# Performance work log

Measured on AMD Instinct MI355X. Metric: run time of the kernel, lower is better.

## Reference

```python
import jax, jax.numpy as jnp
from jax import lax
import numpy as np

AXIS = 16      # axis_neuron
N_TYPES = 2    # number of atom types


def _mlp(x, Ws, bs):
    for W, b in zip(Ws, bs):
        x = jnp.tanh(x @ W + b)
    return x


def _forward(sym, dx, dy, dz, types,
             fw0, fb0, fw1, fb1, fw2, fb2,
             gw0, gb0, gw1, gb1, gw2, gb2, gwo, gbo):
    # sym/dx/dy/dz: (B, N, SEL, 4); types: (B, N) int
    N, SEL = sym.shape[1], sym.shape[2]

    def frame_fn(R, DX, DY, DZ, ty):
        E_atoms = jnp.zeros((N,), R.dtype)
        F = jnp.zeros((N, 3), R.dtype)
        for t in range(N_TYPES):  # loop over small fixed set of atom types
            mask = (ty == t).astype(R.dtype)            # (N,)
            cnt = jnp.maximum(mask.sum(), 1.0)
            m3 = mask[:, None, None]
            sji = R[:, :, 0:1]
            xyz = R[:, :, 1:4]
            ns = cnt * SEL
            nx = ns * 3.0
            s_avg = (sji * m3).sum() / ns
            x_avg = (xyz * m3).sum() / nx
            s_avg2 = ((sji ** 2) * m3).sum() / ns
            x_avg2 = ((xyz ** 2) * m3).sum() / nx
            avg2 = jnp.stack([s_avg2, x_avg2, x_avg2, x_avg2])
            avg1 = jnp.stack([s_avg, x_avg, x_avg, x_avg])
            std = jnp.sqrt(jnp.maximum(avg2 - avg1 ** 2, 0.0)) + 1e-8
            avg = jnp.stack([s_avg, 0.0 * s_avg, 0.0 * s_avg, 0.0 * s_avg])
            avg = lax.stop_gradient(avg)   # torch computes stats under no_grad
            std = lax.stop_gradient(std)
            Rn = (R - avg) / std
            DXn = DX / std
            DYn = DY / std
            DZn = DZ / std

            def etot(Rn_):
                s = Rn_[:, :, 0:1]                                  # (N, SEL, 1)
                G = _mlp(s, [fw0[t], fw1[t], fw2[t]], [fb0[t], fb1[t], fb2[t]])  # (N, SEL, M)
                RG = jnp.einsum('nsf,nsm->nfm', Rn_, G)             # (N, 4, M)
                GRRG = jnp.einsum('nfm,nfa->nma', RG, RG[:, :, :AXIS]).reshape(N, -1)  # (N, M*AXIS)
                denom = cnt * GRRG.shape[1]
                mu = (GRRG * mask[:, None]).sum() / denom
                mu2 = ((GRRG ** 2) * mask[:, None]).sum() / denom
                sd = jnp.sqrt(jnp.maximum(mu2 - mu ** 2, 0.0)) + 1e-8
                h = _mlp((GRRG - mu) / sd,
                         [gw0[t], gw1[t], gw2[t]], [gb0[t], gb1[t], gb2[t]])
                e = (h @ gwo[t] + gbo[t])[:, 0]                     # (N,)
                return (e * mask).sum(), e

            (Et, e_atoms), dR = jax.value_and_grad(etot, has_aux=True)(Rn)
            E_atoms = E_atoms + e_atoms * mask
            Fx = (dR * DXn).sum(axis=(1, 2))
            Fy = (dR * DYn).sum(axis=(1, 2))
            Fz = (dR * DZn).sum(axis=(1, 2))
            # "DO NOT forget to multiply -1 for F!!!"
            F = F - jnp.stack([Fx, Fy, Fz], axis=1) * mask[:, None]
        return E_atoms.sum(), F

    return jax.vmap(frame_fn)(sym, dx, dy, dz, types)


def setup_inputs() -> dict:
    key = jax.random.key(0)
    ks = jax.random.split(key, 24)
    B, N, SEL = 4, 1024, 128
    M = 100                     # filter_neuron[-1]
    FIT_IN = AXIS * M           # 1600
    d = {}
    d['sym'] = jax.random.normal(ks[0], (B, N, SEL, 4), jnp.float32)
    d['dx'] = jax.random.normal(ks[1], (B, N, SEL, 4), jnp.float32)
    d['dy'] = jax.random.normal(ks[2], (B, N, SEL, 4), jnp.float32)
    d['dz'] = jax.random.normal(ks[3], (B, N, SEL, 4), jnp.float32)
    d['types'] = jax.random.randint(ks[4], (B, N), 0, N_TYPES, jnp.int32)

    def w(k, shape):
        return jax.random.normal(k, shape, jnp.float32) / np.float32(np.sqrt(shape[-2]))

    def b(k, shape):
        return 0.1 * jax.random.normal(k, shape, jnp.float32)

    d['fw0'] = w(ks[5], (N_TYPES, 1, 25));      d['fb0'] = b(ks[6], (N_TYPES, 25))
    d['fw1'] = w(ks[7], (N_TYPES, 25, 50));     d['fb1'] = b(ks[8], (N_TYPES, 50))
    d['fw2'] = w(ks[9], (N_TYPES, 50, M));      d['fb2'] = b(ks[10], (N_TYPES, M))
    d['gw0'] = w(ks[11], (N_TYPES, FIT_IN, 240)); d['gb0'] = b(ks[12], (N_TYPES, 240))
    d['gw1'] = w(ks[13], (N_TYPES, 240, 240));  d['gb1'] = b(ks[14], (N_TYPES, 240))
    d['gw2'] = w(ks[15], (N_TYPES, 240, 240));  d['gb2'] = b(ks[16], (N_TYPES, 240))
    d['gwo'] = w(ks[17], (N_TYPES, 240, 1));    d['gbo'] = b(ks[18], (N_TYPES, 1))
    return d


def reference(sym, dx, dy, dz, types,
              fw0, fb0, fw1, fb1, fw2, fb2,
              gw0, gb0, gw1, gb1, gw2, gb2, gwo, gbo):
    return _forward(sym, dx, dy, dz, types,
                    fw0, fb0, fw1, fb1, fw2, fb2,
                    gw0, gb0, gw1, gb1, gw2, gb2, gwo, gbo)
```

## Files before the change

### kernel.cpp

```cpp
#include <hip/hip_runtime.h>

#define NBATCH 4
#define NATOM 1024
#define NSEL 128
#define H1 25
#define H2 50
#define HM 100
#define AX 16
#define GF 1600
#define FI 240
#define NT 2
#define NGRP64 18

#define WS_STATS_RAW 0
#define WS_STATS_FIN 64
#define WS_MUSD_RAW 128
#define WS_MUSD_FIN 144
#define WS_S_RAW 176
#define WS_CTR 192
#define WS_EBUF 256
#define WS_IDX (WS_EBUF + NBATCH*NATOM)
#define WS_G (WS_IDX + NBATCH*1152)
#define WS_P (WS_G + (size_t)NBATCH*NATOM*GF)
#define WS_BP0  (WS_P + (size_t)NBATCH*NATOM*GF)
#define WS_BP1  (WS_BP0 + (size_t)NT*15*50*256)
#define WS_BP2  (WS_BP1 + (size_t)NT*15*8*256)
#define WS_BPT2 (WS_BP2 + (size_t)NT*15*8*256)
#define WS_BPT1 (WS_BPT2 + (size_t)NT*15*8*256)
#define WS_BPT0 (WS_BPT1 + (size_t)NT*15*8*256)
#define WS_FW1T (WS_BPT0 + (size_t)NT*100*8*256)
#define WS_FW2T (WS_FW1T + (size_t)NT*H2*H1)
#define WS_RGB (WS_FW2T + (size_t)NT*HM*H2)
#define WS_GTB (WS_RGB + (size_t)NBATCH*NATOM*HM*4)
#define WS_GTB_UNITS ((size_t)NBATCH*NATOM*(HM/2)*NSEL)
#define WS_BF1B  (WS_GTB + WS_GTB_UNITS)
#define WS_BW2TB (WS_BF1B + (size_t)NT*1024)
#define WS_BW1TB (WS_BW2TB + (size_t)NT*4096)
#define WS_BF2B  (WS_BW1TB + (size_t)NT*1024)
#define WS_END   (WS_BF2B + (size_t)NT*3584)

#define GSTR 108

typedef __attribute__((ext_vector_type(8))) short bf16x8;
typedef __attribute__((ext_vector_type(4))) float f32x4;

__device__ __forceinline__ float ftanh(float x){
  float e = __expf(2.0f*x);
  return 1.0f - 2.0f/(e+1.0f);
}
__device__ __forceinline__ unsigned short f2bf(float x){
  unsigned b=__float_as_uint(x); b += 0x7FFF + ((b>>16)&1); return (unsigned short)(b>>16);
}
__device__ __forceinline__ float bf2f(unsigned short h){ return __uint_as_float(((unsigned)h)<<16); }
__device__ __forceinline__ float bflo(unsigned u){ return __uint_as_float(u<<16); }
__device__ __forceinline__ float bfhi(unsigned u){ return __uint_as_float(u & 0xFFFF0000u); }
__device__ __forceinline__ unsigned packbf(float a, float b){
  return (unsigned)f2bf(a) | ((unsigned)f2bf(b)<<16);
}

__device__ __forceinline__ float wave_sum(float v){
#pragma unroll
  for(int o=32;o>0;o>>=1) v += __shfl_down(v,o,64);
  return v;
}
__device__ __forceinline__ float block_sum2(float v, float* red){
  v = wave_sum(v);
  __syncthreads();
  if((threadIdx.x&63)==0) red[threadIdx.x>>6]=v;
  __syncthreads();
  return red[0]+red[1];
}
__device__ __forceinline__ float block_sum4(float v, float* red){
  v = wave_sum(v);
  __syncthreads();
  if((threadIdx.x&63)==0) red[threadIdx.x>>6]=v;
  __syncthreads();
  return red[0]+red[1]+red[2]+red[3];
}

__global__ void __launch_bounds__(256) k_transpose(const float* __restrict__ gw0,
    const float* __restrict__ gw1, const float* __restrict__ gw2,
    const float* __restrict__ fw1, const float* __restrict__ fw2, float* __restrict__ ws){
  const int cB0 = NT*15*50*256;
  const int cB1 = NT*15*8*256;
  const int cT0 = NT*100*8*256;
  const int c6 = NT*H2*H1, c7 = NT*HM*H2;
  const int total = cB0 + 4*cB1 + cT0 + c6 + c7;
  unsigned* wsu = (unsigned*)ws;
  for(int i = blockIdx.x*blockDim.x + threadIdx.x; i < total; i += gridDim.x*blockDim.x){
    if(i < cB0 + 4*cB1 + cT0){
      int base, NKs; const float* W; int KK; int mode; int t;
      int ii = i;
      if(ii < cB0){ base=WS_BP0; NKs=50; KK=1600; mode=0; t = ii/(15*50*256); ii -= t*(15*50*256); W = gw0 + (size_t)t*GF*FI; }
      else if(ii < cB0+cB1){ ii-=cB0; base=WS_BP1; NKs=8; KK=240; mode=0; t = ii/(15*8*256); ii -= t*(15*8*256); W = gw1 + t*FI*FI; }
      else if(ii < cB0+2*cB1){ ii-=cB0+cB1; base=WS_BP2; NKs=8; KK=240; mode=0; t = ii/(15*8*256); ii -= t*(15*8*256); W = gw2 + t*FI*FI; }
      else if(ii < cB0+3*cB1){ ii-=cB0+2*cB1; base=WS_BPT2; NKs=8; KK=240; mode=1; t = ii/(15*8*256); ii -= t*(15*8*256); W = gw2 + t*FI*FI; }
      else if(ii < cB0+4*cB1){ ii-=cB0+3*cB1; base=WS_BPT1; NKs=8; KK=240; mode=1; t = ii/(15*8*256); ii -= t*(15*8*256); W = gw1 + t*FI*FI; }
      else { ii-=cB0+4*cB1; base=WS_BPT0; NKs=8; KK=240; mode=2; t = ii/(100*8*256); ii -= t*(100*8*256); W = gw0 + (size_t)t*GF*FI; }
      int d = ii & 3;
      int lane = (ii>>2) & 63;
      int rem = ii >> 8;
      int ks = rem % NKs;
      int ntile = rem / NKs;
      int n = ntile*16 + (lane&15);
      int k0 = ks*32 + ((lane>>4)&3)*8 + 2*d;
      float v0, v1;
      if(mode==0){
        v0 = (k0   < KK) ? W[(size_t)(k0  )*FI + n] : 0.f;
        v1 = (k0+1 < KK) ? W[(size_t)(k0+1)*FI + n] : 0.f;
      } else if(mode==1){
        v0 = (k0   < KK) ? W[n*FI + k0  ] : 0.f;
        v1 = (k0+1 < KK) ? W[n*FI + k0+1] : 0.f;
      } else {
        v0 = (k0   < KK) ? W[(size_t)n*FI + k0  ] : 0.f;
        v1 = (k0+1 < KK) ? W[(size_t)n*FI + k0+1] : 0.f;
      }
      int telems = (base==WS_BP0) ? 15*50*256 : (base==WS_BPT0 ? 100*8*256 : 15*8*256);
      wsu[base + (size_t)t*telems + ii] = packbf(v0, v1);
    } else if(i < cB0 + 4*cB1 + cT0 + c6){
      int ii = i - (cB0+4*cB1+cT0); int t = ii/(H2*H1); int rem = ii - t*(H2*H1);
      int j = rem/H1; int k = rem - j*H1;
      ws[WS_FW1T + ii] = fw1[t*H1*H2 + k*H2 + j];
    } else {
      int ii = i - (cB0+4*cB1+cT0+c6); int t = ii/(HM*H2); int rem = ii - t*(HM*H2);
      int m = rem/H2; int j = rem - m*H2;
      ws[WS_FW2T + ii] = fw2[t*H2*HM + j*HM + m];
    }
  }
}

__global__ void __launch_bounds__(256) k_packf(const float* __restrict__ fw1,
    const float* __restrict__ fw2, float* __restrict__ ws){
  unsigned* wsu = (unsigned*)ws;
  const int c1 = NT*1024, c2 = NT*4096, c3 = NT*1024, c4 = NT*3584;
  const int total = c1 + c2 + c3 + c4;
  for(int i = blockIdx.x*blockDim.x + threadIdx.x; i < total; i += gridDim.x*blockDim.x){
    if(i < c1){
      int t = i/1024; int ii = i - t*1024;
      int nt = ii>>8; int lane = (ii>>2)&63; int d = ii&3;
      int n = nt*16 + (lane&15);
      int k0 = ((lane>>4)&3)*8 + 2*d;
      float v0 = (k0   < H1 && n < H2) ? fw1[t*H1*H2 + (k0  )*H2 + n] : 0.f;
      float v1 = (k0+1 < H1 && n < H2) ? fw1[t*H1*H2 + (k0+1)*H2 + n] : 0.f;
      wsu[WS_BF1B + i] = packbf(v0, v1);
    } else if(i < c1 + c2){
      int ii = i - c1; int t = ii/4096; ii -= t*4096;
      int nt = ii>>10; int ks = (ii>>8)&3; int lane = (ii>>2)&63; int d = ii&3;
      int n = nt*16 + (lane&15);
      int k0 = ks*32 + ((lane>>4)&3)*8 + 2*d;
      float v0 = (k0   < HM && n < H2) ? fw2[t*H2*HM + n*HM + k0  ] : 0.f;
      float v1 = (k0+1 < HM && n < H2) ? fw2[t*H2*HM + n*HM + k0+1] : 0.f;
      wsu[WS_BW2TB + ii + t*4096] = packbf(v0, v1);
    } else if(i < c1 + c2 + c3){
      int ii = i - c1 - c2; int t = ii/1024; ii -= t*1024;
      int nt = ii>>9; int ks = (ii>>8)&1; int lane = (ii>>2)&63; int d = ii&3;
      int n = nt*16 + (lane&15);
      int k0 = ks*32 + ((lane>>4)&3)*8 + 2*d;
      float v0 = (k0   < H2 && n < H1) ? fw1[t*H1*H2 + n*H2 + k0  ] : 0.f;
      float v1 = (k0+1 < H2 && n < H1) ? fw1[t*H1*H2 + n*H2 + k0+1] : 0.f;
      wsu[WS_BW1TB + ii + t*1024] = packbf(v0, v1);
    } else {
      int ii = i - c1 - c2 - c3; int t = ii/3584; ii -= t*3584;
      int nt = ii>>9; int ks = (ii>>8)&1; int lane = (ii>>2)&63; int d = ii&3;
      int n = nt*16 + (lane&15);
      int k0 = ks*32 + ((lane>>4)&3)*8 + 2*d;
      float v0 = (k0   < H2 && n < HM) ? fw2[t*H2*HM + (k0  )*HM + n] : 0.f;
      float v1 = (k0+1 < H2 && n < HM) ? fw2[t*H2*HM + (k0+1)*HM + n] : 0.f;
      wsu[WS_BF2B + ii + t*3584] = packbf(v0, v1);
    }
  }
}

__global__ void __launch_bounds__(256) k_stats(const float* __restrict__ sym,
    const int* __restrict__ types, float* __restrict__ ws){
  const int b = blockIdx.y;
  const int n0 = blockIdx.x * 64;
  const float* R = sym + ((size_t)b*NATOM + n0)*NSEL*4;
  const int* ty = types + b*NATOM;
  float ss0=0,ss20=0,xs0=0,xs20=0,ss1=0,ss21=0,xs1=0,xs21=0,c0=0,c1=0;
  for(int idx=threadIdx.x; idx<64*NSEL*4; idx+=256){
    int a = idx >> 9;
    int t = ty[n0+a];
    float v = R[idx];
    bool iss = (idx&3)==0;
    if(t==0){ if(iss){ss0+=v;ss20+=v*v;} else {xs0+=v;xs20+=v*v;} }
    else    { if(iss){ss1+=v;ss21+=v*v;} else {xs1+=v;xs21+=v*v;} }
  }
  if(threadIdx.x<64){ if(ty[n0+threadIdx.x]==0) c0=1.f; else c1=1.f; }
  ss0=wave_sum(ss0); ss20=wave_sum(ss20); xs0=wave_sum(xs0); xs20=wave_sum(xs20); c0=wave_sum(c0);
  ss1=wave_sum(ss1); ss21=wave_sum(ss21); xs1=wave_sum(xs1); xs21=wave_sum(xs21); c1=wave_sum(c1);
  if((threadIdx.x&63)==0){
    float* r0 = ws + WS_STATS_RAW + (b*2+0)*8;
    float* r1 = ws + WS_STATS_RAW + (b*2+1)*8;
    atomicAdd(r0+0,c0); atomicAdd(r0+1,ss0); atomicAdd(r0+2,ss20); atomicAdd(r0+3,xs0); atomicAdd(r0+4,xs20);
    atomicAdd(r1+0,c1); atomicAdd(r1+1,ss1); atomicAdd(r1+2,ss21); atomicAdd(r1+3,xs1); atomicAdd(r1+4,xs21);
  }
}

__global__ void k_fin_stats(float* ws){
  int i = threadIdx.x;
  if(i<8){
    float* raw = ws + WS_STATS_RAW + i*8;
    float cntf = fmaxf(raw[0], 1.f);
    float ns = cntf * (float)NSEL;
    float s_avg = raw[1]/ns, s_avg2 = raw[2]/ns;
    float x_avg = raw[3]/(ns*3.f), x_avg2 = raw[4]/(ns*3.f);
    float std_s = sqrtf(fmaxf(s_avg2 - s_avg*s_avg, 0.f)) + 1e-8f;
    float std_x = sqrtf(fmaxf(x_avg2 - x_avg*x_avg, 0.f)) + 1e-8f;
    float* fin = ws + WS_STATS_FIN + i*8;
    fin[0]=s_avg; fin[1]=1.f/std_s; fin[2]=1.f/std_x; fin[3]=cntf; fin[4]=raw[0];
  }
}

__global__ void k_index(const int* __restrict__ types, float* __restrict__ ws){
  int b = blockIdx.x;
  int rc0 = (int)ws[WS_STATS_FIN + (b*2)*8 + 4];
  int pad0 = (rc0+63)&~63;
  int* ctr = (int*)ws + WS_CTR;
  int* idx = (int*)ws + WS_IDX;
  for(int n=threadIdx.x;n<NATOM;n+=256){
    int t = types[b*NATOM+n];
    int pos = atomicAdd(&ctr[b*2+t],1);
    idx[b*1152 + (t ? pad0+pos : pos)] = n;
  }
}

__global__ void __launch_bounds__(128) k_fwdm(const float* __restrict__ sym, const int* __restrict__ types,
    const float* __restrict__ fw0,const float* __restrict__ fb0,
    const float* __restrict__ fb1,const float* __restrict__ fb2,
    float* __restrict__ ws){
  extern __shared__ char fraw[];
  float* Rn4 = (float*)fraw;
  float* RG4 = (float*)(fraw + 2048);
  float* red = (float*)(fraw + 3648);
  unsigned short* a2F = (unsigned short*)(fraw + 3680);
  unsigned* a2Fu = (unsigned*)(fraw + 3680);
  unsigned* a1L = (unsigned*)(fraw + 20576);
  unsigned short* Gl = (unsigned short*)(fraw + 20576);

  const int bid = blockIdx.x;
  const int b = bid >> 10;
  int t = types[bid];
  t = __builtin_amdgcn_readfirstlane(t);
  const float* fin = ws + WS_STATS_FIN + (b*2+t)*8;
  const float avg_s = fin[0], inv_ss = fin[1], inv_sx = fin[2];
  const int s = threadIdx.x;
  const int wave = s>>6, lane = s&63, lw = lane&15, lg = lane>>4;

  const float* W0 = fw0 + t*H1; const float* B0 = fb0 + t*H1;
  const float* B1 = fb1 + t*H2; const float* B2 = fb2 + t*HM;
  const unsigned* wsu = (const unsigned*)ws;
  const bf16x8* BF1 = (const bf16x8*)(wsu + WS_BF1B) + t*4*64;
  const bf16x8* BF2 = (const bf16x8*)(wsu + WS_BF2B) + t*14*64;

  float4 R4 = *(const float4*)&sym[(size_t)bid*NSEL*4 + s*4];
  float rn0 = (R4.x-avg_s)*inv_ss, rn1 = R4.y*inv_sx, rn2 = R4.z*inv_sx, rn3 = R4.w*inv_sx;
  *(float4*)&Rn4[s*4] = make_float4(rn0,rn1,rn2,rn3);

  {
    float a1r[H1];
#pragma unroll
    for(int kk=0;kk<H1;kk++) a1r[kk] = ftanh(rn0*W0[kk] + B0[kk]);
    unsigned* rw = a1L + s*17;
#pragma unroll
    for(int q=0;q<12;q++) rw[q] = packbf(a1r[2*q], a1r[2*q+1]);
    rw[12] = packbf(a1r[24], 0.f);
    rw[13]=0; rw[14]=0; rw[15]=0; rw[16]=0;
  }
  __syncthreads();

  const f32x4 fz = {0.f,0.f,0.f,0.f};
  for(int nt=0;nt<4;nt++){
    f32x4 acc[4];
#pragma unroll
    for(int mt=0;mt<4;mt++){
      int MT = wave*4 + mt;
      bf16x8 af = *(const bf16x8*)&a1L[(MT*16+lw)*17 + lg*4];
      acc[mt] = __builtin_amdgcn_mfma_f32_16x16x32_bf16(af, BF1[nt*64+lane], fz, 0,0,0);
    }
    int col = nt*16 + lw;
    float bias = (col<H2) ? B1[col] : 0.f;
#pragma unroll
    for(int mt=0;mt<4;mt++)
#pragma unroll
      for(int r=0;r<4;r++){
        int rw = (wave*4+mt)*16 + lg*4 + r;
        float v = (col<H2) ? ftanh(acc[mt][r] + bias) : 0.f;
        a2F[rw*66 + col] = f2bf(v);
      }
  }
  __syncthreads();
  for(int nt=0;nt<7;nt++){
    f32x4 acc[4];
#pragma unroll
    for(int mt=0;mt<4;mt++) acc[mt] = fz;
    for(int ks=0;ks<2;ks++){
#pragma unroll
      for(int mt=0;mt<4;mt++){
        int MT = wave*4 + mt;
        bf16x8 af = *(const bf16x8*)&a2Fu[(MT*16+lw)*33 + ks*16 + lg*4];
        acc[mt] = __builtin_amdgcn_mfma_f32_16x16x32_bf16(af, BF2[(nt*2+ks)*64+lane], acc[mt], 0,0,0);
      }
    }
    int col = nt*16 + lw;
    if(col < HM){
      float bias = B2[col];
#pragma unroll
      for(int mt=0;mt<4;mt++)
#pragma unroll
        for(int r=0;r<4;r++){
          int rw = (wave*4+mt)*16 + lg*4 + r;
          Gl[rw*GSTR + col] = f2bf(ftanh(acc[mt][r] + bias));
        }
    }
  }
  __syncthreads();
  if(s < HM){
    const int m = s;
    float a0=0,b0=0,c0=0,d0=0;
    for(int sn=0;sn<NSEL;sn++){
      float4 rn = *(const float4*)&Rn4[sn*4];
      float g = bf2f(Gl[sn*GSTR+m]);
      a0 += rn.x*g; b0 += rn.y*g; c0 += rn.z*g; d0 += rn.w*g;
    }
    *(float4*)&RG4[m*4] = make_float4(a0,b0,c0,d0);
  }
  __syncthreads();
  for(int i=s;i<HM*4;i+=128) ws[WS_RGB + (size_t)bid*(HM*4) + i] = RG4[i];
  {
    unsigned* GT = (unsigned*)ws + WS_GTB + (size_t)bid*((HM/2)*NSEL);
    for(int i=s;i<(HM/2)*NSEL;i+=128){
      int mp = i >> 7, ss = i & 127;
      GT[i] = *(const unsigned*)&Gl[ss*GSTR + 2*mp];
    }
  }
  float lsum=0,lsum2=0;
  float* gout = ws + WS_G + (size_t)bid*GF;
  for(int i=s;i<GF;i+=128){
    int m=i>>4, a=i&15;
    float4 rm = *(const float4*)&RG4[m*4];
    float4 ra = *(const float4*)&RG4[a*4];
    float gv = rm.x*ra.x + rm.y*ra.y + rm.z*ra.z + rm.w*ra.w;
    gout[i]=gv; lsum+=gv; lsum2+=gv*gv;
  }
  lsum = block_sum2(lsum, red);
  lsum2 = block_sum2(lsum2, red);
  if(s==0){
    atomicAdd(&ws[WS_MUSD_RAW + (b*2+t)*2 + 0], lsum);
    atomicAdd(&ws[WS_MUSD_RAW + (b*2+t)*2 + 1], lsum2);
  }
}

__global__ void __launch_bounds__(128) k_fwd(const float* __restrict__ sym, const int* __restrict__ types,
    const float* __restrict__ fw0,const float* __restrict__ fb0,
    const float* __restrict__ fb1,const float* __restrict__ fb2,
    float* __restrict__ ws){
  __shared__ float Rn4[NSEL*4];
  __shared__ unsigned short Gl[NSEL*GSTR];
  __shared__ float RG4[HM*4];
  __shared__ float red[8];

  const int bid = blockIdx.x;
  const int b = bid >> 10;
  int t = types[bid];
  t = __builtin_amdgcn_readfirstlane(t);
  const float* fin = ws + WS_STATS_FIN + (b*2+t)*8;
  const float avg_s = fin[0], inv_ss = fin[1], inv_sx = fin[2];
  const int s = threadIdx.x;

  const float* W0 = fw0 + t*H1; const float* B0 = fb0 + t*H1;
  const float* B1 = fb1 + t*H2; const float* B2 = fb2 + t*HM;
  const float* W1T = ws + WS_FW1T + t*H2*H1;
  const float* W2T = ws + WS_FW2T + t*HM*H2;

  float4 R4 = *(const float4*)&sym[(size_t)bid*NSEL*4 + s*4];
  float rn0 = (R4.x-avg_s)*inv_ss, rn1 = R4.y*inv_sx, rn2 = R4.z*inv_sx, rn3 = R4.w*inv_sx;
  *(float4*)&Rn4[s*4] = make_float4(rn0,rn1,rn2,rn3);

  float a1[H1];
#pragma unroll
  for(int k=0;k<H1;k++) a1[k] = ftanh(rn0*W0[k] + B0[k]);
  float a2[H2];
#pragma unroll
  for(int j=0;j<H2;j++){
    float acc = B1[j];
    const float* wr = W1T + j*H1;
#pragma unroll
    for(int k=0;k<H1;k++) acc += a1[k]*wr[k];
    a2[j] = ftanh(acc);
  }
  for(int m=0;m<HM;m+=4){
    const float* wr0 = W2T + m*H2; const float* wr1 = wr0 + H2;
    const float* wr2 = wr1 + H2;  const float* wr3 = wr2 + H2;
    float acc0 = B2[m], acc1 = B2[m+1], acc2 = B2[m+2], acc3 = B2[m+3];
#pragma unroll
    for(int j=0;j<H2;j++){
      float aj = a2[j];
      acc0 += aj*wr0[j]; acc1 += aj*wr1[j]; acc2 += aj*wr2[j]; acc3 += aj*wr3[j];
    }
    unsigned u0 = (unsigned)f2bf(ftanh(acc0)) | ((unsigned)f2bf(ftanh(acc1))<<16);
    unsigned u1 = (unsigned)f2bf(ftanh(acc2)) | ((unsigned)f2bf(ftanh(acc3))<<16);
    *(unsigned*)&Gl[s*GSTR + m] = u0;
    *(unsigned*)&Gl[s*GSTR + m + 2] = u1;
  }
  __syncthreads();
  if(s < HM){
    const int m = s;
    float a0=0,b0=0,c0=0,d0=0;
    for(int sn=0;sn<NSEL;sn++){
      float4 rn = *(const float4*)&Rn4[sn*4];
      float g = bf2f(Gl[sn*GSTR+m]);
      a0 += rn.x*g; b0 += rn.y*g; c0 += rn.z*g; d0 += rn.w*g;
    }
    *(float4*)&RG4[m*4] = make_float4(a0,b0,c0,d0);
  }
  __syncthreads();
  for(int i=s;i<HM*4;i+=128) ws[WS_RGB + (size_t)bid*(HM*4) + i] = RG4[i];
  float lsum=0,lsum2=0;
  float* gout = ws + WS_G + (size_t)bid*GF;
  for(int i=s;i<GF;i+=128){
    int m=i>>4, a=i&15;
    float4 rm = *(const float4*)&RG4[m*4];
    float4 ra = *(const float4*)&RG4[a*4];
    float gv = rm.x*ra.x + rm.y*ra.y + rm.z*ra.z + rm.w*ra.w;
    gout[i]=gv; lsum+=gv; lsum2+=gv*gv;
  }
  lsum = block_sum2(lsum, red);
  lsum2 = block_sum2(lsum2, red);
  if(s==0){
    atomicAdd(&ws[WS_MUSD_RAW + (b*2+t)*2 + 0], lsum);
    atomicAdd(&ws[WS_MUSD_RAW + (b*2+t)*2 + 1], lsum2);
  }
}

__global__ void k_fin_musd(float* ws){
  int i=threadIdx.x;
  if(i<8){
    float cntf = ws[WS_STATS_FIN + i*8 + 3];
    float denom = cntf * (float)GF;
    float Sg = ws[WS_MUSD_RAW + i*2], Sg2 = ws[WS_MUSD_RAW + i*2+1];
    float mu = Sg/denom, mu2 = Sg2/denom;
    float var = fmaxf(mu2 - mu*mu, 0.f);
    float r = sqrtf(var); float sd = r + 1e-8f;
    float* mf = ws + WS_MUSD_FIN + i*4;
    mf[0]=mu; mf[1]=1.f/sd; mf[2]=r; mf[3]=sd;
  }
}

__global__ void __launch_bounds__(256) k_fitm(
    const float* __restrict__ gb0,const float* __restrict__ gb1,
    const float* __restrict__ gb2,
    const float* __restrict__ gwo,const float* __restrict__ gbo,
    float* __restrict__ ws){
  extern __shared__ unsigned short lb[];
  unsigned short* h1S = lb;
  unsigned short* h2S = lb + 16896;
  unsigned short* dzA = lb + 33792;
  __shared__ float red[4];

  const int b = blockIdx.x / NGRP64;
  const int grp = blockIdx.x - b*NGRP64;
  int rc0 = (int)ws[WS_STATS_FIN + (b*2)*8 + 4];
  int rc1 = (int)ws[WS_STATS_FIN + (b*2+1)*8 + 4];
  rc0 = __builtin_amdgcn_readfirstlane(rc0);
  rc1 = __builtin_amdgcn_readfirstlane(rc1);
  const int pad0 = (rc0+63)&~63;
  const int tend = pad0 + ((rc1+63)&~63);
  const int slot0 = grp*64;
  if(slot0 >= tend) return;
  const int t = (slot0 >= pad0) ? 1 : 0;

  const float* mf = ws + WS_MUSD_FIN + (b*2+t)*4;
  const float mu = mf[0], isd = mf[1];

  const int tid = threadIdx.x;
  const int wave = tid>>6, lane = tid&63;
  const int lw = lane&15, lg = lane>>4;
  const int mRowBase = wave*16 + lg*4;

  const int* idx = (const int*)ws + WS_IDX + b*1152;
  int arow = idx[slot0 + wave*16 + lw];
  int rowSafe = arow<0?0:arow;
  const float* yrowA = ws + WS_G + (size_t)(b*NATOM + rowSafe)*GF;
  int idC[4];
#pragma unroll
  for(int r=0;r<4;r++) idC[r] = idx[slot0 + wave*16 + lg*4 + r];

  const unsigned* wsu = (const unsigned*)ws;
  const bf16x8* BP0  = (const bf16x8*)(wsu + WS_BP0)  + (size_t)t*15*50*64;
  const bf16x8* BP1  = (const bf16x8*)(wsu + WS_BP1)  + t*15*8*64;
  const bf16x8* BP2  = (const bf16x8*)(wsu + WS_BP2)  + t*15*8*64;
  const bf16x8* BPT2 = (const bf16x8*)(wsu + WS_BPT2) + t*15*8*64;
  const bf16x8* BPT1 = (const bf16x8*)(wsu + WS_BPT1) + t*15*8*64;
  const bf16x8* BPT0 = (const bf16x8*)(wsu + WS_BPT0) + (size_t)t*100*8*64;

  for(int i=tid;i<64*24;i+=256){
    int r = i/24, c = 240 + (i - (i/24)*24);
    h1S[r*264+c]=0; h2S[r*264+c]=0; dzA[r*264+c]=0;
  }

  f32x4 acc[15];
  const f32x4 fz = {0.f,0.f,0.f,0.f};
#pragma unroll
  for(int nt=0;nt<15;nt++) acc[nt] = fz;
  for(int ks=0;ks<50;ks++){
    float4 y0 = *(const float4*)(yrowA + ks*32 + lg*8);
    float4 y1 = *(const float4*)(yrowA + ks*32 + lg*8 + 4);
    union{ unsigned u[4]; bf16x8 v; } A;
    A.u[0]=packbf((y0.x-mu)*isd,(y0.y-mu)*isd); A.u[1]=packbf((y0.z-mu)*isd,(y0.w-mu)*isd);
    A.u[2]=packbf((y1.x-mu)*isd,(y1.y-mu)*isd); A.u[3]=packbf((y1.z-mu)*isd,(y1.w-mu)*isd);
#pragma unroll
    for(int nt=0;nt<15;nt++)
      acc[nt] = __builtin_amdgcn_mfma_f32_16x16x32_bf16(A.v, BP0[(nt*50+ks)*64+lane], acc[nt], 0,0,0);
  }
#pragma unroll
  for(int nt=0;nt<15;nt++){
    float bias = gb0[t*FI + nt*16 + lw];
#pragma unroll
    for(int r=0;r<4;r++){
      float h = ftanh(acc[nt][r] + bias);
      h1S[(mRowBase+r)*264 + nt*16 + lw] = f2bf(h);
    }
  }
  __syncthreads();
#pragma unroll
  for(int nt=0;nt<15;nt++) acc[nt] = fz;
  for(int ks=0;ks<8;ks++){
    bf16x8 a = *(const bf16x8*)&h1S[(wave*16+lw)*264 + ks*32 + lg*8];
#pragma unroll
    for(int nt=0;nt<15;nt++)
      acc[nt] = __builtin_amdgcn_mfma_f32_16x16x32_bf16(a, BP1[(nt*8+ks)*64+lane], acc[nt], 0,0,0);
  }
#pragma unroll
  for(int nt=0;nt<15;nt++){
    float bias = gb1[t*FI + nt*16 + lw];
#pragma unroll
    for(int r=0;r<4;r++){
      float h = ftanh(acc[nt][r] + bias);
      h2S[(mRowBase+r)*264 + nt*16 + lw] = f2bf(h);
    }
  }
  __syncthreads();
#pragma unroll
  for(int nt=0;nt<15;nt++) acc[nt] = fz;
  for(int ks=0;ks<8;ks++){
    bf16x8 a = *(const bf16x8*)&h2S[(wave*16+lw)*264 + ks*32 + lg*8];
#pragma unroll
    for(int nt=0;nt<15;nt++)
      acc[nt] = __builtin_amdgcn_mfma_f32_16x16x32_bf16(a, BP2[(nt*8+ks)*64+lane], acc[nt], 0,0,0);
  }
  float pe[4] = {0.f,0.f,0.f,0.f};
#pragma unroll
  for(int nt=0;nt<15;nt++){
    float bias = gb2[t*FI + nt*16 + lw];
    float wo = gwo[t*FI + nt*16 + lw];
#pragma unroll
    for(int r=0;r<4;r++){
      float h = ftanh(acc[nt][r] + bias);
      pe[r] += h*wo;
      float d3 = wo*(1.f - h*h);
      dzA[(mRowBase+r)*264 + nt*16 + lw] = f2bf(d3);
    }
  }
#pragma unroll
  for(int o=1;o<16;o<<=1){
#pragma unroll
    for(int r=0;r<4;r++) pe[r] += __shfl_xor(pe[r], o, 64);
  }
  if(lw==0){
#pragma unroll
    for(int r=0;r<4;r++) if(idC[r]>=0) ws[WS_EBUF + b*NATOM + idC[r]] = pe[r] + gbo[t];
  }
  __syncthreads();
#pragma unroll
  for(int nt=0;nt<15;nt++) acc[nt] = fz;
  for(int ks=0;ks<8;ks++){
    bf16x8 a = *(const bf16x8*)&dzA[(wave*16+lw)*264 + ks*32 + lg*8];
#pragma unroll
    for(int nt=0;nt<15;nt++)
      acc[nt] = __builtin_amdgcn_mfma_f32_16x16x32_bf16(a, BPT2[(nt*8+ks)*64+lane], acc[nt], 0,0,0);
  }
#pragma unroll
  for(int nt=0;nt<15;nt++){
#pragma unroll
    for(int r=0;r<4;r++){
      float h2 = bf2f(h2S[(mRowBase+r)*264 + nt*16 + lw]);
      acc[nt][r] *= (1.f - h2*h2);
    }
  }
  __syncthreads();
#pragma unroll
  for(int nt=0;nt<15;nt++){
#pragma unroll
    for(int r=0;r<4;r++) dzA[(mRowBase+r)*264 + nt*16 + lw] = f2bf(acc[nt][r]);
  }
  __syncthreads();
#pragma unroll
  for(int nt=0;nt<15;nt++) acc[nt] = fz;
  for(int ks=0;ks<8;ks++){
    bf16x8 a = *(const bf16x8*)&dzA[(wave*16+lw)*264 + ks*32 + lg*8];
#pragma unroll
    for(int nt=0;nt<15;nt++)
      acc[nt] = __builtin_amdgcn_mfma_f32_16x16x32_bf16(a, BPT1[(nt*8+ks)*64+lane], acc[nt], 0,0,0);
  }
#pragma unroll
  for(int nt=0;nt<15;nt++){
#pragma unroll
    for(int r=0;r<4;r++){
      float h1 = bf2f(h1S[(mRowBase+r)*264 + nt*16 + lw]);
      acc[nt][r] *= (1.f - h1*h1);
    }
  }
  __syncthreads();
#pragma unroll
  for(int nt=0;nt<15;nt++){
#pragma unroll
    for(int r=0;r<4;r++) dzA[(mRowBase+r)*264 + nt*16 + lw] = f2bf(acc[nt][r]);
  }
  __syncthreads();
  const float* yG = ws + WS_G + (size_t)b*NATOM*GF;
  float* pP = ws + WS_P + (size_t)b*NATOM*GF;
  float s1t=0.f, syt=0.f;
  for(int c0=0;c0<100;c0+=10){
    f32x4 pc[10];
#pragma unroll
    for(int j=0;j<10;j++) pc[j] = fz;
    for(int ks=0;ks<8;ks++){
      bf16x8 a = *(const bf16x8*)&dzA[(wave*16+lw)*264 + ks*32 + lg*8];
#pragma unroll
      for(int j=0;j<10;j++)
        pc[j] = __builtin_amdgcn_mfma_f32_16x16x32_bf16(a, BPT0[((c0+j)*8+ks)*64+lane], pc[j], 0,0,0);
    }
#pragma unroll
    for(int j=0;j<10;j++){
      int n = (c0+j)*16 + lw;
#pragma unroll
      for(int r=0;r<4;r++){
        if(idC[r]>=0){
          float pv = pc[j][r];
          size_t off = (size_t)idC[r]*GF + n;
          pP[off] = pv;
          s1t += pv;
          syt += pv * (yG[off]-mu)*isd;
        }
      }
    }
  }
  s1t = block_sum4(s1t, red);
  syt = block_sum4(syt, red);
  if(tid==0){
    atomicAdd(&ws[WS_S_RAW+(b*2+t)*2+0], s1t);
    atomicAdd(&ws[WS_S_RAW+(b*2+t)*2+1], syt);
  }
}

__global__ void __launch_bounds__(128) k_bwdm2(const float* __restrict__ sym,
    const float* __restrict__ dxp,const float* __restrict__ dyp,const float* __restrict__ dzp,
    const int* __restrict__ types,
    const float* __restrict__ fw0,const float* __restrict__ fb0,
    const float* __restrict__ fb1,
    float* __restrict__ ws, float* __restrict__ out){
  extern __shared__ char lraw[];
  float* dRG4 = (float*)lraw;
  unsigned* a1L = (unsigned*)(lraw + 1600);
  float* red = (float*)(lraw + 10304);
  float* dgb = (float*)(lraw + 10368);
  float* RG4 = (float*)(lraw + 17168);
  unsigned short* a2L = (unsigned short*)(lraw + 10368);
  unsigned short* dz2s = (unsigned short*)(lraw + 26752);
  unsigned* dz2u = (unsigned*)(lraw + 26752);
  unsigned* dz3L = (unsigned*)(lraw + 43648);
  unsigned short* dz1L = (unsigned short*)(lraw + 43648);

  const int bid = blockIdx.x;
  const int b = bid >> 10;
  int t = types[bid];
  t = __builtin_amdgcn_readfirstlane(t);
  const float* fin = ws + WS_STATS_FIN + (b*2+t)*8;
  const float avg_s=fin[0], inv_ss=fin[1], inv_sx=fin[2], cntf=fin[3];
  const float* mf = ws + WS_MUSD_FIN + (b*2+t)*4;
  const float mu=mf[0], inv_sd=mf[1], rr=mf[2];
  const float S1 = ws[WS_S_RAW + (b*2+t)*2 + 0];
  const float Sy = ws[WS_S_RAW + (b*2+t)*2 + 1];
  const float denom = cntf * (float)GF;
  const float c1 = S1/denom;
  const float c2 = (rr>0.f) ? (Sy/denom)/rr : 0.f;
  const int s = threadIdx.x;
  const int wave = s>>6, lane = s&63, lw = lane&15, lg = lane>>4;

  const float* W0 = fw0 + t*H1; const float* B0 = fb0 + t*H1;
  const float* B1f = fb1 + t*H2;
  const unsigned* wsu = (const unsigned*)ws;
  const bf16x8* BF1  = (const bf16x8*)(wsu + WS_BF1B)  + t*4*64;
  const bf16x8* BW2T = (const bf16x8*)(wsu + WS_BW2TB) + t*16*64;
  const bf16x8* BW1T = (const bf16x8*)(wsu + WS_BW1TB) + t*4*64;

  for(int i=s;i<HM*4;i+=128) RG4[i] = ws[WS_RGB + (size_t)bid*(HM*4) + i];
  __syncthreads();
  const float* p = ws + WS_P + (size_t)bid*GF;
  for(int i=s;i<GF;i+=128){
    int m=i>>4, a=i&15;
    float4 rm = *(const float4*)&RG4[m*4];
    float4 ra = *(const float4*)&RG4[a*4];
    float gv = rm.x*ra.x + rm.y*ra.y + rm.z*ra.z + rm.w*ra.w;
    float yv = (gv-mu)*inv_sd;
    dgb[m*17+a] = (p[i]-c1)*inv_sd - yv*c2;
  }
  __syncthreads();
  if(s < HM){
    const int m = s;
    float a0=0,b0=0,c0=0,d0=0;
#pragma unroll
    for(int a=0;a<AX;a++){
      float d = dgb[m*17+a];
      float4 r = *(const float4*)&RG4[a*4];
      a0 += d*r.x; b0 += d*r.y; c0 += d*r.z; d0 += d*r.w;
    }
    if(m<AX){
      for(int mp=0;mp<HM;mp++){
        float d = dgb[mp*17+m];
        float4 r = *(const float4*)&RG4[mp*4];
        a0 += d*r.x; b0 += d*r.y; c0 += d*r.z; d0 += d*r.w;
      }
    }
    *(float4*)&dRG4[m*4] = make_float4(a0,b0,c0,d0);
  }
  float4 R4 = *(const float4*)&sym[(size_t)bid*NSEL*4 + s*4];
  float rn0 = (R4.x-avg_s)*inv_ss, rn1 = R4.y*inv_sx, rn2 = R4.z*inv_sx, rn3 = R4.w*inv_sx;
  {
    float a1r[H1];
#pragma unroll
    for(int kk=0;kk<H1;kk++) a1r[kk] = ftanh(rn0*W0[kk] + B0[kk]);
    unsigned* row = a1L + s*17;
#pragma unroll
    for(int q=0;q<12;q++) row[q] = packbf(a1r[2*q], a1r[2*q+1]);
    row[12] = packbf(a1r[24], 0.f);
    row[13]=0; row[14]=0; row[15]=0; row[16]=0;
  }
  __syncthreads();

  const f32x4 fz = {0.f,0.f,0.f,0.f};
  for(int nt=0;nt<4;nt++){
    f32x4 acc[4];
#pragma unroll
    for(int mt=0;mt<4;mt++){
      bf16x8 af = *(const bf16x8*)&a1L[((wave*4+mt)*16+lw)*17 + lg*4];
      acc[mt] = __builtin_amdgcn_mfma_f32_16x16x32_bf16(af, BF1[nt*64+lane], fz, 0,0,0);
    }
    int col = nt*16 + lw;
    float bias = (col<H2) ? B1f[col] : 0.f;
#pragma unroll
    for(int mt=0;mt<4;mt++)
#pragma unroll
      for(int r=0;r<4;r++){
        int rw = (wave*4+mt)*16 + lg*4 + r;
        a2L[rw*64 + col] = f2bf(ftanh(acc[mt][r] + bias));
      }
  }
  const unsigned* GT = (const unsigned*)ws + WS_GTB + (size_t)bid*((HM/2)*NSEL);
  float drn0=0,drn1=0,drn2=0,drn3=0;
  {
    unsigned* row = dz3L + s*65;
    for(int q=0;q<50;q++){
      int m0 = 2*q;
      unsigned u = GT[q*NSEL + s];
      float g0 = bflo(u), g1 = bfhi(u);
      float4 dm0 = *(const float4*)&dRG4[m0*4];
      float4 dm1 = *(const float4*)&dRG4[(m0+1)*4];
      drn0 += dm0.x*g0 + dm1.x*g1;
      drn1 += dm0.y*g0 + dm1.y*g1;
      drn2 += dm0.z*g0 + dm1.z*g1;
      drn3 += dm0.w*g0 + dm1.w*g1;
      float d30 = (dm0.x*rn0 + dm0.y*rn1 + dm0.z*rn2 + dm0.w*rn3)*(1.f-g0*g0);
      float d31 = (dm1.x*rn0 + dm1.y*rn1 + dm1.z*rn2 + dm1.w*rn3)*(1.f-g1*g1);
      row[q] = packbf(d30, d31);
    }
#pragma unroll
    for(int q=50;q<64;q++) row[q] = 0;
  }
  __syncthreads();
  for(int nt=0;nt<4;nt++){
    f32x4 acc[4];
#pragma unroll
    for(int mt=0;mt<4;mt++) acc[mt] = fz;
    for(int ks=0;ks<4;ks++){
#pragma unroll
      for(int mt=0;mt<4;mt++){
        bf16x8 af = *(const bf16x8*)&dz3L[((wave*4+mt)*16+lw)*65 + ks*16 + lg*4];
        acc[mt] = __builtin_amdgcn_mfma_f32_16x16x32_bf16(af, BW2T[(nt*4+ks)*64+lane], acc[mt], 0,0,0);
      }
    }
    int col = nt*16 + lw;
#pragma unroll
    for(int mt=0;mt<4;mt++)
#pragma unroll
      for(int r=0;r<4;r++){
        int rw = (wave*4+mt)*16 + lg*4 + r;
        float a2v = bf2f(a2L[rw*64 + col]);
        dz2s[rw*66 + col] = f2bf(acc[mt][r]*(1.f - a2v*a2v));
      }
  }
  __syncthreads();
  for(int nt2=0;nt2<2;nt2++){
    f32x4 acc[4];
#pragma unroll
    for(int mt=0;mt<4;mt++) acc[mt] = fz;
    for(int ks2=0;ks2<2;ks2++){
#pragma unroll
      for(int mt=0;mt<4;mt++){
        bf16x8 af = *(const bf16x8*)&dz2u[((wave*4+mt)*16+lw)*33 + ks2*16 + lg*4];
        acc[mt] = __builtin_amdgcn_mfma_f32_16x16x32_bf16(af, BW1T[(nt2*2+ks2)*64+lane], acc[mt], 0,0,0);
      }
    }
    int col = nt2*16 + lw;
    if(col < 28){
#pragma unroll
      for(int mt=0;mt<4;mt++)
#pragma unroll
        for(int r=0;r<4;r++){
          int rw = (wave*4+mt)*16 + lg*4 + r;
          dz1L[rw*28 + col] = f2bf((col<H1) ? acc[mt][r] : 0.f);
        }
    }
  }
  __syncthreads();
  {
    const unsigned short* a1s = (const unsigned short*)a1L;
    float ds = 0.f;
#pragma unroll
    for(int kk=0;kk<H1;kk++){
      float d1 = bf2f(dz1L[s*28 + kk]);
      float a1v = bf2f(a1s[s*34 + kk]);
      ds += d1*(1.f - a1v*a1v)*W0[kk];
    }
    drn0 += ds;
  }
  float w0 = drn0*inv_ss, w1 = drn1*inv_sx, w2 = drn2*inv_sx, w3 = drn3*inv_sx;
  float4 X = *(const float4*)&dxp[(size_t)bid*NSEL*4 + s*4];
  float4 Y = *(const float4*)&dyp[(size_t)bid*NSEL*4 + s*4];
  float4 Z = *(const float4*)&dzp[(size_t)bid*NSEL*4 + s*4];
  float fx = w0*X.x + w1*X.y + w2*X.z + w3*X.w;
  float fy = w0*Y.x + w1*Y.y + w2*Y.z + w3*Y.w;
  float fz2 = w0*Z.x + w1*Z.y + w2*Z.z + w3*Z.w;
  fx = wave_sum(fx); fy = wave_sum(fy); fz2 = wave_sum(fz2);
  __syncthreads();
  if((s&63)==0){ int w=s>>6; red[w*3+0]=fx; red[w*3+1]=fy; red[w*3+2]=fz2; }
  __syncthreads();
  if(s==0){
    float* F = out + 4 + (size_t)bid*3;
    F[0] = -(red[0]+red[3]);
    F[1] = -(red[1]+red[4]);
    F[2] = -(red[2]+red[5]);
  }
}

__global__ void __launch_bounds__(128) k_bwd0(const float* __restrict__ sym,
    const float* __restrict__ dxp,const float* __restrict__ dyp,const float* __restrict__ dzp,
    const int* __restrict__ types,
    const float* __restrict__ fw0,const float* __restrict__ fb0,
    const float* __restrict__ fw1,const float* __restrict__ fb1,
    const float* __restrict__ fb2,
    float* __restrict__ ws, float* __restrict__ out){
  __shared__ float RG4[HM*4];
  __shared__ float dgb[HM*17];
  __shared__ float dRG4[HM*4];
  __shared__ float red[8];

  const int bid = blockIdx.x;
  const int b = bid >> 10;
  int t = types[bid];
  t = __builtin_amdgcn_readfirstlane(t);
  const float* fin = ws + WS_STATS_FIN + (b*2+t)*8;
  const float avg_s=fin[0], inv_ss=fin[1], inv_sx=fin[2], cntf=fin[3];
  const float* mf = ws + WS_MUSD_FIN + (b*2+t)*4;
  const float mu=mf[0], inv_sd=mf[1], rr=mf[2];
  const float S1 = ws[WS_S_RAW + (b*2+t)*2 + 0];
  const float Sy = ws[WS_S_RAW + (b*2+t)*2 + 1];
  const float denom = cntf * (float)GF;
  const float c1 = S1/denom;
  const float c2 = (rr>0.f) ? (Sy/denom)/rr : 0.f;
  const int s = threadIdx.x;

  const float* W0 = fw0 + t*H1; const float* B0 = fb0 + t*H1;
  const float* B1 = fb1 + t*H2; const float* B2 = fb2 + t*HM;
  const float* W1  = fw1 + t*H1*H2;
  const float* W1T = ws + WS_FW1T + t*H2*H1;
  const float* W2T = ws + WS_FW2T + t*HM*H2;

  for(int i=s;i<HM*4;i+=128) RG4[i] = ws[WS_RGB + (size_t)bid*(HM*4) + i];
  __syncthreads();

  const float* p = ws + WS_P + (size_t)bid*GF;
  for(int i=s;i<GF;i+=128){
    int m=i>>4, a=i&15;
    float4 rm = *(const float4*)&RG4[m*4];
    float4 ra = *(const float4*)&RG4[a*4];
    float gv = rm.x*ra.x + rm.y*ra.y + rm.z*ra.z + rm.w*ra.w;
    float yv = (gv-mu)*inv_sd;
    dgb[m*17+a] = (p[i]-c1)*inv_sd - yv*c2;
  }
  __syncthreads();
  if(s < HM){
    const int m = s;
    float a0=0,b0=0,c0=0,d0=0;
#pragma unroll
    for(int a=0;a<AX;a++){
      float d = dgb[m*17+a];
      float4 r = *(const float4*)&RG4[a*4];
      a0 += d*r.x; b0 += d*r.y; c0 += d*r.z; d0 += d*r.w;
    }
    if(m<AX){
      for(int mp=0;mp<HM;mp++){
        float d = dgb[mp*17+m];
        float4 r = *(const float4*)&RG4[mp*4];
        a0 += d*r.x; b0 += d*r.y; c0 += d*r.z; d0 += d*r.w;
      }
    }
    *(float4*)&dRG4[m*4] = make_float4(a0,b0,c0,d0);
  }
  __syncthreads();

  float4 R4 = *(const float4*)&sym[(size_t)bid*NSEL*4 + s*4];
  float rn0 = (R4.x-avg_s)*inv_ss, rn1 = R4.y*inv_sx, rn2 = R4.z*inv_sx, rn3 = R4.w*inv_sx;

  float a1[H1];
#pragma unroll
  for(int kk=0;kk<H1;kk++) a1[kk] = ftanh(rn0*W0[kk] + B0[kk]);
  float a2[H2];
#pragma unroll
  for(int j=0;j<H2;j++){
    float acc = B1[j];
    const float* wr = W1T + j*H1;
#pragma unroll
    for(int kk=0;kk<H1;kk++) acc += a1[kk]*wr[kk];
    a2[j] = ftanh(acc);
  }

  float dz2a[H2];
#pragma unroll
  for(int j=0;j<H2;j++) dz2a[j]=0.f;
  float drn0=0,drn1=0,drn2=0,drn3=0;
  for(int m=0;m<HM;m+=4){
    const float* wr0 = W2T + m*H2; const float* wr1 = wr0 + H2;
    const float* wr2 = wr1 + H2;  const float* wr3 = wr2 + H2;
    float acc0 = B2[m], acc1 = B2[m+1], acc2 = B2[m+2], acc3 = B2[m+3];
#pragma unroll
    for(int j=0;j<H2;j++){
      float aj = a2[j];
      acc0 += aj*wr0[j]; acc1 += aj*wr1[j]; acc2 += aj*wr2[j]; acc3 += aj*wr3[j];
    }
    float g0 = ftanh(acc0), g1 = ftanh(acc1), g2 = ftanh(acc2), g3 = ftanh(acc3);
    float4 d0 = *(const float4*)&dRG4[m*4];
    float4 d1 = *(const float4*)&dRG4[(m+1)*4];
    float4 d2 = *(const float4*)&dRG4[(m+2)*4];
    float4 d3 = *(const float4*)&dRG4[(m+3)*4];
    drn0 += d0.x*g0 + d1.x*g1 + d2.x*g2 + d3.x*g3;
    drn1 += d0.y*g0 + d1.y*g1 + d2.y*g2 + d3.y*g3;
    drn2 += d0.z*g0 + d1.z*g1 + d2.z*g2 + d3.z*g3;
    drn3 += d0.w*g0 + d1.w*g1 + d2.w*g2 + d3.w*g3;
    float dz30 = (d0.x*rn0 + d0.y*rn1 + d0.z*rn2 + d0.w*rn3)*(1.f-g0*g0);
    float dz31 = (d1.x*rn0 + d1.y*rn1 + d1.z*rn2 + d1.w*rn3)*(1.f-g1*g1);
    float dz32 = (d2.x*rn0 + d2.y*rn1 + d2.z*rn2 + d2.w*rn3)*(1.f-g2*g2);
    float dz33 = (d3.x*rn0 + d3.y*rn1 + d3.z*rn2 + d3.w*rn3)*(1.f-g3*g3);
#pragma unroll
    for(int j=0;j<H2;j++) dz2a[j] += dz30*wr0[j] + dz31*wr1[j] + dz32*wr2[j] + dz33*wr3[j];
  }
#pragma unroll
  for(int j=0;j<H2;j++){ float av=a2[j]; dz2a[j] *= (1.f-av*av); }
  float dsacc=0.f;
#pragma unroll
  for(int kk=0;kk<H1;kk++){
    const float* wr = W1 + kk*H2;
    float acc=0.f;
#pragma unroll
    for(int j=0;j<H2;j++) acc += dz2a[j]*wr[j];
    float av=a1[kk];
    dsacc += acc*(1.f-av*av)*W0[kk];
  }
  drn0 += dsacc;
  float w0 = drn0*inv_ss, w1 = drn1*inv_sx, w2 = drn2*inv_sx, w3 = drn3*inv_sx;
  float4 X = *(const float4*)&dxp[(size_t)bid*NSEL*4 + s*4];
  float4 Y = *(const float4*)&dyp[(size_t)bid*NSEL*4 + s*4];
  float4 Z = *(const float4*)&dzp[(size_t)bid*NSEL*4 + s*4];
  float fx = w0*X.x + w1*X.y + w2*X.z + w3*X.w;
  float fy = w0*Y.x + w1*Y.y + w2*Y.z + w3*Y.w;
  float fz = w0*Z.x + w1*Z.y + w2*Z.z + w3*Z.w;
  fx = wave_sum(fx); fy = wave_sum(fy); fz = wave_sum(fz);
  __syncthreads();
  if((s&63)==0){ int w=s>>6; red[w*3+0]=fx; red[w*3+1]=fy; red[w*3+2]=fz; }
  __syncthreads();
  if(s==0){
    float* F = out + 4 + (size_t)bid*3;
    F[0] = -(red[0]+red[3]);
    F[1] = -(red[1]+red[4]);
    F[2] = -(red[2]+red[5]);
  }
}

__global__ void k_write_E(const float* __restrict__ ws, float* __restrict__ out){
  __shared__ float red[8];
  const int b = blockIdx.x;
  const float* e = ws + WS_EBUF + b*NATOM;
  float sv=0;
  for(int i=threadIdx.x;i<NATOM;i+=256) sv+=e[i];
  sv = block_sum4(sv, red);
  if(threadIdx.x==0) out[b]=sv;
}

extern "C" void kernel_launch(void* const* d_in, const int* in_sizes, int n_in,
                              void* d_out, int out_size, void* d_ws, size_t ws_size,
                              hipStream_t stream) {
  const float* sym = (const float*)d_in[0];
  const float* dxp = (const float*)d_in[1];
  const float* dyp = (const float*)d_in[2];
  const float* dzp = (const float*)d_in[3];
  const int*   types=(const int*)d_in[4];
  const float* fw0=(const float*)d_in[5];
  const float* fb0=(const float*)d_in[6];
  const float* fw1=(const float*)d_in[7];
  const float* fb1=(const float*)d_in[8];
  const float* fw2=(const float*)d_in[9];
  const float* fb2=(const float*)d_in[10];
  const float* gw0=(const float*)d_in[11];
  const float* gb0=(const float*)d_in[12];
  const float* gw1=(const float*)d_in[13];
  const float* gb1=(const float*)d_in[14];
  const float* gw2=(const float*)d_in[15];
  const float* gb2=(const float*)d_in[16];
  const float* gwo=(const float*)d_in[17];
  const float* gbo=(const float*)d_in[18];
  float* ws = (float*)d_ws;
  float* out = (float*)d_out;

  const size_t need_bytes = (size_t)WS_END * 4;
  const int storeGT = (ws_size >= need_bytes) ? 1 : 0;

  hipMemsetAsync(d_ws, 0, 1024, stream);
  hipMemsetAsync((char*)d_ws + (size_t)WS_IDX*4, 0xFF, (size_t)NBATCH*1152*4, stream);

  k_transpose<<<1024,256,0,stream>>>(gw0,gw1,gw2,fw1,fw2,ws);
  if(storeGT) k_packf<<<64,256,0,stream>>>(fw1,fw2,ws);
  k_stats<<<dim3(16,NBATCH),256,0,stream>>>(sym,types,ws);
  k_fin_stats<<<1,64,0,stream>>>(ws);
  k_index<<<NBATCH,256,0,stream>>>(types,ws);

  if(storeGT){
    const int lds_fwdm = 48224;
    hipFuncSetAttribute((const void*)k_fwdm, hipFuncAttributeMaxDynamicSharedMemorySize, lds_fwdm);
    k_fwdm<<<NBATCH*NATOM,128,lds_fwdm,stream>>>(sym,types,fw0,fb0,fb1,fb2,ws);
  } else {
    k_fwd<<<NBATCH*NATOM,128,0,stream>>>(sym,types,fw0,fb0,fb1,fb2,ws);
  }
  k_fin_musd<<<1,64,0,stream>>>(ws);

  const int lds_fitm = 3*64*264*2;
  hipFuncSetAttribute((const void*)k_fitm, hipFuncAttributeMaxDynamicSharedMemorySize, lds_fitm);
  k_fitm<<<NBATCH*NGRP64,256,lds_fitm,stream>>>(gb0,gb1,gb2,gwo,gbo,ws);

  if(storeGT){
    const int lds_bwdm = 76928;
    hipFuncSetAttribute((const void*)k_bwdm2, hipFuncAttributeMaxDynamicSharedMemorySize, lds_bwdm);
    k_bwdm2<<<NBATCH*NATOM,128,lds_bwdm,stream>>>(sym,dxp,dyp,dzp,types,fw0,fb0,fb1,ws,out);
  } else {
    k_bwd0<<<NBATCH*NATOM,128,0,stream>>>(sym,dxp,dyp,dzp,types,fw0,fb0,fw1,fb1,fb2,ws,out);
  }

  k_write_E<<<NBATCH,256,0,stream>>>(ws,out);
}
```

Baseline: 856.0 us.

## Stream dz3 K-slices through a small LDS buffer in backward MLP kernel

Instead of materializing the full 128x64 bf16 dz3 matrix in LDS before the MFMA pass, the backward kernel now builds one 16-column K-slice at a time and accumulates all four N-tiles in registers across slices. This cuts the LDS footprint of k_bwdm2 from about 77KB to 52KB so more blocks can be resident per CU. The cost is 64 accumulator registers per thread and two extra barriers per K-step, which may raise register pressure and add synchronization.

Measured after the change: 907.1 us. 6.0% more time.

```diff
diff --git a/kernel.cpp b/kernel.cpp
--- a/kernel.cpp
+++ b/kernel.cpp
@@ -669,7 +669,7 @@
   unsigned short* a2L = (unsigned short*)(lraw + 10368);
   unsigned short* dz2s = (unsigned short*)(lraw + 26752);
   unsigned* dz2u = (unsigned*)(lraw + 26752);
-  unsigned* dz3L = (unsigned*)(lraw + 43648);
+  unsigned* AL = (unsigned*)(lraw + 43648);
   unsigned short* dz1L = (unsigned short*)(lraw + 43648);
 
   const int bid = blockIdx.x;
@@ -759,37 +759,47 @@
   }
   const unsigned* GT = (const unsigned*)ws + WS_GTB + (size_t)bid*((HM/2)*NSEL);
   float drn0=0,drn1=0,drn2=0,drn3=0;
-  {
-    unsigned* row = dz3L + s*65;
-    for(int q=0;q<50;q++){
-      int m0 = 2*q;
-      unsigned u = GT[q*NSEL + s];
-      float g0 = bflo(u), g1 = bfhi(u);
-      float4 dm0 = *(const float4*)&dRG4[m0*4];
-      float4 dm1 = *(const float4*)&dRG4[(m0+1)*4];
-      drn0 += dm0.x*g0 + dm1.x*g1;
-      drn1 += dm0.y*g0 + dm1.y*g1;
-      drn2 += dm0.z*g0 + dm1.z*g1;
-      drn3 += dm0.w*g0 + dm1.w*g1;
-      float d30 = (dm0.x*rn0 + dm0.y*rn1 + dm0.z*rn2 + dm0.w*rn3)*(1.f-g0*g0);
-      float d31 = (dm1.x*rn0 + dm1.y*rn1 + dm1.z*rn2 + dm1.w*rn3)*(1.f-g1*g1);
-      row[q] = packbf(d30, d31);
-    }
-#pragma unroll
-    for(int q=50;q<64;q++) row[q] = 0;
-  }
-  __syncthreads();
+  f32x4 accD[4][4];
+#pragma unroll
+  for(int nt=0;nt<4;nt++)
+#pragma unroll
+    for(int mt=0;mt<4;mt++) accD[nt][mt] = fz;
+  for(int ks=0;ks<4;ks++){
+    {
+      unsigned* row = AL + s*17;
+#pragma unroll
+      for(int mlp=0;mlp<16;mlp++){
+        int q = ks*16 + mlp;
+        float d30=0.f, d31=0.f;
+        if(q < 50){
+          int m0 = 2*q;
+          unsigned u = GT[q*NSEL + s];
+          float g0 = bflo(u), g1 = bfhi(u);
+          float4 dm0 = *(const float4*)&dRG4[m0*4];
+          float4 dm1 = *(const float4*)&dRG4[(m0+1)*4];
+          drn0 += dm0.x*g0 + dm1.x*g1;
+          drn1 += dm0.y*g0 + dm1.y*g1;
+          drn2 += dm0.z*g0 + dm1.z*g1;
+          drn3 += dm0.w*g0 + dm1.w*g1;
+          d30 = (dm0.x*rn0 + dm0.y*rn1 + dm0.z*rn2 + dm0.w*rn3)*(1.f-g0*g0);
+          d31 = (dm1.x*rn0 + dm1.y*rn1 + dm1.z*rn2 + dm1.w*rn3)*(1.f-g1*g1);
+        }
+        row[mlp] = packbf(d30, d31);
+      }
+    }
+    __syncthreads();
+#pragma unroll
+    for(int nt=0;nt<4;nt++){
+#pragma unroll
+      for(int mt=0;mt<4;mt++){
+        bf16x8 af = *(const bf16x8*)&AL[((wave*4+mt)*16+lw)*17 + lg*4];
+        accD[nt][mt] = __builtin_amdgcn_mfma_f32_16x16x32_bf16(af, BW2T[(nt*4+ks)*64+lane], accD[nt][mt], 0,0,0);
+      }
+    }
+    __syncthreads();
+  }
+#pragma unroll
   for(int nt=0;nt<4;nt++){
-    f32x4 acc[4];
-#pragma unroll
-    for(int mt=0;mt<4;mt++) acc[mt] = fz;
-    for(int ks=0;ks<4;ks++){
-#pragma unroll
-      for(int mt=0;mt<4;mt++){
-        bf16x8 af = *(const bf16x8*)&dz3L[((wave*4+mt)*16+lw)*65 + ks*16 + lg*4];
-        acc[mt] = __builtin_amdgcn_mfma_f32_16x16x32_bf16(af, BW2T[(nt*4+ks)*64+lane], acc[mt], 0,0,0);
-      }
-    }
     int col = nt*16 + lw;
 #pragma unroll
     for(int mt=0;mt<4;mt++)
@@ -797,7 +807,7 @@
       for(int r=0;r<4;r++){
         int rw = (wave*4+mt)*16 + lg*4 + r;
         float a2v = bf2f(a2L[rw*64 + col]);
-        dz2s[rw*66 + col] = f2bf(acc[mt][r]*(1.f - a2v*a2v));
+        dz2s[rw*66 + col] = f2bf(accD[nt][mt][r]*(1.f - a2v*a2v));
       }
   }
   __syncthreads();
@@ -1058,7 +1068,7 @@
   k_fitm<<<NBATCH*NGRP64,256,lds_fitm,stream>>>(gb0,gb1,gb2,gwo,gbo,ws);
 
   if(storeGT){
-    const int lds_bwdm = 76928;
+    const int lds_bwdm = 52352;
     hipFuncSetAttribute((const void*)k_bwdm2, hipFuncAttributeMaxDynamicSharedMemorySize, lds_bwdm);
     k_bwdm2<<<NBATCH*NATOM,128,lds_bwdm,stream>>>(sym,dxp,dyp,dzp,types,fw0,fb0,fb1,ws,out);
   } else {
```
